# Kernel optimization log

Measured on AMD Instinct MI355X. Metric: run time of the kernel, lower is better.

Reference implementation:

```python
import jax, jax.numpy as jnp
import numpy as np

N = 20000      # vertices
KPV = 8        # key points per vertex
M = N * KPV    # total key points
E = 320000     # edges (avg in-degree 16)
KP_DIM = 4
SD = 300       # state_dim
T = 3          # GNN iterations
NC = 4         # classes
LOC = (64, 64, 7)


def _lin(key, din, dout):
    k1, k2 = jax.random.split(key)
    s = 1.0 / np.sqrt(din)
    W = jax.random.uniform(k1, (din, dout), jnp.float32, -s, s)
    b = jax.random.uniform(k2, (dout,), jnp.float32, -s, s)
    return W, b


def setup_inputs():
    key = jax.random.key(0)
    ks = jax.random.split(key, 32)
    inp = {}
    inp['key_points'] = jax.random.normal(ks[0], (M, KP_DIM), jnp.float32)
    inp['pos'] = jax.random.normal(ks[1], (N, 3), jnp.float32)
    # uniform ragged layout: vertex i owns key points [i*KPV, (i+1)*KPV)
    inp['key_points_lookup'] = jnp.arange(N, dtype=jnp.int32) * KPV
    inp['edge_index'] = jax.random.randint(ks[2], (2, E), 0, N, jnp.int32)
    # MLPInit: kp_dim -> 64 -> 128 -> state_dim (basic_block = Linear+ReLU)
    inp['Wi0'], inp['bi0'] = _lin(ks[3], KP_DIM, 64)
    inp['Wi1'], inp['bi1'] = _lin(ks[4], 64, 128)
    inp['Wi2'], inp['bi2'] = _lin(ks[5], 128, SD)
    # MLPInitAggr: state_dim -> state_dim
    inp['Wa'], inp['ba'] = _lin(ks[6], SD, SD)
    # StateConvLayer params per iteration (mlp_h: s->delta_x, mlp_f: [dx,s_j]->e, mlp_g: update)
    Wh, bh, Wf, bf, Wg, bg = [], [], [], [], [], []
    for t in range(T):
        w, b = _lin(ks[7 + 3 * t], SD, 3); Wh.append(w); bh.append(b)
        w, b = _lin(ks[8 + 3 * t], SD + 3, SD); Wf.append(w); bf.append(b)
        w, b = _lin(ks[9 + 3 * t], SD, SD); Wg.append(w); bg.append(b)
    inp['Wh'] = jnp.stack(Wh); inp['bh'] = jnp.stack(bh)
    inp['Wf'] = jnp.stack(Wf); inp['bf'] = jnp.stack(bf)
    inp['Wg'] = jnp.stack(Wg); inp['bg'] = jnp.stack(bg)
    # classification head: state_dim -> 64 -> n_classes
    inp['Wc1'], inp['bc1'] = _lin(ks[16], SD, 64)
    inp['Wc2'], inp['bc2'] = _lin(ks[17], 64, NC)
    # per-class localization heads: state_dim -> 64 -> 64 -> 7 (stacked over classes)
    Wl1, bl1, Wl2, bl2, Wl3, bl3 = [], [], [], [], [], []
    for c in range(NC):
        w, b = _lin(ks[18 + 3 * c], SD, LOC[0]); Wl1.append(w); bl1.append(b)
        w, b = _lin(ks[19 + 3 * c], LOC[0], LOC[1]); Wl2.append(w); bl2.append(b)
        w, b = _lin(ks[20 + 3 * c], LOC[1], LOC[2]); Wl3.append(w); bl3.append(b)
    inp['Wl1'] = jnp.stack(Wl1); inp['bl1'] = jnp.stack(bl1)
    inp['Wl2'] = jnp.stack(Wl2); inp['bl2'] = jnp.stack(bl2)
    inp['Wl3'] = jnp.stack(Wl3); inp['bl3'] = jnp.stack(bl3)
    return inp


def reference(key_points, pos, key_points_lookup, edge_index,
              Wi0, bi0, Wi1, bi1, Wi2, bi2, Wa, ba,
              Wh, bh, Wf, bf, Wg, bg,
              Wc1, bc1, Wc2, bc2,
              Wl1, bl1, Wl2, bl2, Wl3, bl3):
    relu = jax.nn.relu
    n = pos.shape[0]
    # ---- initial vertex state: per-key-point MLP + ragged segment-max ----
    feats = relu(key_points @ Wi0 + bi0)
    feats = relu(feats @ Wi1 + bi1)
    feats = relu(feats @ Wi2 + bi2)                      # [M, SD]
    seg = jnp.searchsorted(key_points_lookup,
                           jnp.arange(feats.shape[0], dtype=jnp.int32),
                           side='right') - 1              # key point -> vertex id
    kp_max = jax.ops.segment_max(feats, seg, num_segments=n)  # [N, SD]
    s = relu(kp_max @ Wa + ba)                            # initial vertex states
    # ---- GNN iterations (Point-GNN eqns, max aggregation) ----
    src, dst = edge_index[0], edge_index[1]
    for t in range(Wh.shape[0]):
        dx = s @ Wh[t] + bh[t]                            # [N, 3] predicted offset
        m = jnp.concatenate([pos[src] - pos[dst] + dx[dst], s[src]], axis=-1)
        e = relu(m @ Wf[t] + bf[t])                       # [E, SD] edge messages
        aggr = jax.ops.segment_max(e, dst, num_segments=n)
        aggr = jnp.where(jnp.isneginf(aggr), 0.0, aggr)   # empty segments -> 0
        s = s + (aggr @ Wg[t] + bg[t])                    # residual state update
    # ---- heads ----
    cls_pred = relu(relu(s @ Wc1 + bc1) @ Wc2 + bc2)      # [N, NC]
    h = relu(jnp.einsum('nd,cdk->cnk', s, Wl1) + bl1[:, None, :])
    h = relu(jnp.einsum('cnd,cdk->cnk', h, Wl2) + bl2[:, None, :])
    h = relu(jnp.einsum('cnd,cdk->cnk', h, Wl3) + bl3[:, None, :])  # [C, N, 7]
    reg_pred = jnp.transpose(h, (1, 0, 2)).reshape(n, -1)           # [N, C*7]
    return cls_pred, reg_pred
```

## Files before the change

kernel.cpp:

```cpp
#include <hip/hip_runtime.h>
#include <stdint.h>

#define N_V   20000
#define M_KP  160000
#define E_N   320000
#define SD    300
#define T_IT  3

typedef unsigned short bf16_t;
typedef __attribute__((ext_vector_type(8))) short short8_t;
typedef __attribute__((ext_vector_type(4))) float float4_t;

__device__ __forceinline__ float bf2f(bf16_t u) {
    return __uint_as_float(((unsigned)u) << 16);
}
__device__ __forceinline__ bf16_t f2bf(float f) {
    unsigned u = __float_as_uint(f);
    unsigned r = (u + 0x7FFFu + ((u >> 16) & 1u)) >> 16;
    return (bf16_t)r;
}

template<bool F32>
__device__ __forceinline__ float LD(const void* p, size_t i) {
    if (F32) return ((const float*)p)[i];
    return bf2f(((const bf16_t*)p)[i]);
}
template<bool F32>
__device__ __forceinline__ void ST(void* p, size_t i, float v) {
    if (F32) ((float*)p)[i] = v;
    else     ((bf16_t*)p)[i] = f2bf(v);
}
__device__ __forceinline__ float LDr(const void* p, long long i, bool f32) {
    return f32 ? ((const float*)p)[i] : bf2f(((const bf16_t*)p)[i]);
}
__device__ __forceinline__ void STr(void* p, size_t i, float v, bool f32) {
    if (f32) ((float*)p)[i] = v;
    else     ((bf16_t*)p)[i] = f2bf(v);
}

__global__ void k_detect(const unsigned* __restrict__ w, int* __restrict__ flag) {
    __shared__ int cnt_s;
    if (threadIdx.x == 0) cnt_s = 0;
    __syncthreads();
    unsigned u = w[threadIdx.x];
    unsigned lo = u & 0xFFFFu;
    int e = (lo >> 7) & 0xFF;
    int plaus = (lo == 0u) || (e >= 96 && e <= 126);
    atomicAdd(&cnt_s, plaus);
    __syncthreads();
    if (threadIdx.x == 0) flag[0] = (cnt_s >= 64) ? 0 : 1;
}

__global__ void k_zero(int* p, int n) {
    int i = blockIdx.x * blockDim.x + threadIdx.x;
    if (i < n) p[i] = 0;
}
__global__ void k_hist(const int* __restrict__ dst, int* __restrict__ cnt) {
    int e = blockIdx.x * blockDim.x + threadIdx.x;
    if (e < E_N) atomicAdd(&cnt[dst[e]], 1);
}
__global__ void k_scan(const int* __restrict__ cnt, int* __restrict__ offs,
                       int* __restrict__ cur) {
    __shared__ int buf[1024];
    __shared__ int carry_s;
    int tid = threadIdx.x;
    if (tid == 0) { carry_s = 0; offs[0] = 0; }
    __syncthreads();
    for (int base = 0; base < N_V; base += 1024) {
        int i = base + tid;
        int v = (i < N_V) ? cnt[i] : 0;
        buf[tid] = v;
        __syncthreads();
        for (int off = 1; off < 1024; off <<= 1) {
            int t = (tid >= off) ? buf[tid - off] : 0;
            __syncthreads();
            buf[tid] += t;
            __syncthreads();
        }
        int incl = buf[tid] + carry_s;
        if (i < N_V) { offs[i + 1] = incl; cur[i] = incl - v; }
        __syncthreads();
        if (tid == 1023) carry_s = incl;
        __syncthreads();
    }
}
__global__ void k_scatter(const int* __restrict__ src, const int* __restrict__ dst,
                          int* __restrict__ cur, int* __restrict__ esrc) {
    int e = blockIdx.x * blockDim.x + threadIdx.x;
    if (e < E_N) {
        int p = atomicAdd(&cur[dst[e]], 1);
        esrc[p] = src[e];
    }
}

template<bool F32>
__global__ __launch_bounds__(256) void k_init_fused(
    const void* __restrict__ kp,
    const void* __restrict__ Wi0, const void* __restrict__ bi0,
    const void* __restrict__ Wi1, const void* __restrict__ bi1,
    const void* __restrict__ Wi2, const void* __restrict__ bi2,
    float* __restrict__ kpmax, const int* __restrict__ flag) {
    if ((flag[0] != 0) != F32) return;
    __shared__ float kps[256];
    __shared__ float h1s[64][64];
    __shared__ float h2s[64 * 128];
    int tid = threadIdx.x;
    int row0 = blockIdx.x * 64;
    kps[tid] = LD<F32>(kp, (size_t)row0 * 4 + tid);
    __syncthreads();
    {
        int c = tid & 63;
        float w0 = LD<F32>(Wi0, c), w1 = LD<F32>(Wi0, 64 + c);
        float w2 = LD<F32>(Wi0, 128 + c), w3 = LD<F32>(Wi0, 192 + c);
        float b0 = LD<F32>(bi0, c);
        int rbase = (tid >> 6) * 16;
#pragma unroll
        for (int rr = 0; rr < 16; rr++) {
            int r = rbase + rr;
            float a = b0 + kps[r * 4] * w0 + kps[r * 4 + 1] * w1
                         + kps[r * 4 + 2] * w2 + kps[r * 4 + 3] * w3;
            h1s[r][c] = fmaxf(a, 0.f);
        }
    }
    __syncthreads();
    {
        int c = tid & 127;
        int rbase = (tid >> 7) * 32;
        float b1 = LD<F32>(bi1, c);
        float acc[32];
#pragma unroll
        for (int rr = 0; rr < 32; rr++) acc[rr] = b1;
        for (int k = 0; k < 64; k++) {
            float wv = LD<F32>(Wi1, (size_t)k * 128 + c);
#pragma unroll
            for (int rr = 0; rr < 32; rr++) acc[rr] += h1s[rbase + rr][k] * wv;
        }
#pragma unroll
        for (int rr = 0; rr < 32; rr++)
            h2s[(size_t)(rbase + rr) * 128 + c] = fmaxf(acc[rr], 0.f);
    }
    __syncthreads();
    {
        int cx = tid & 63, rg = tid >> 6;
        float acc[16][5];
#pragma unroll
        for (int r = 0; r < 16; r++)
#pragma unroll
            for (int j = 0; j < 5; j++) acc[r][j] = 0.f;
        bool ok4 = (cx < SD - 256);
        for (int k = 0; k < 128; k++) {
            float w[5];
#pragma unroll
            for (int j = 0; j < 4; j++) w[j] = LD<F32>(Wi2, (size_t)k * SD + cx + 64 * j);
            w[4] = ok4 ? LD<F32>(Wi2, (size_t)k * SD + cx + 256) : 0.f;
#pragma unroll
            for (int r = 0; r < 16; r++) {
                float av = h2s[(rg * 16 + r) * 128 + k];
#pragma unroll
                for (int j = 0; j < 5; j++) acc[r][j] += av * w[j];
            }
        }
        int vbase = (row0 >> 3) + rg * 2;
#pragma unroll
        for (int half = 0; half < 2; half++) {
            int v = vbase + half;
#pragma unroll
            for (int j = 0; j < 5; j++) {
                int c = cx + 64 * j;
                if (c >= SD) continue;
                float m = acc[half * 8][j];
#pragma unroll
                for (int r = 1; r < 8; r++) m = fmaxf(m, acc[half * 8 + r][j]);
                kpmax[(size_t)v * SD + c] = fmaxf(m + LD<F32>(bi2, c), 0.f);
            }
        }
    }
}

template<bool F32>
__global__ __launch_bounds__(256) void k_gemm(
    const float* __restrict__ A, const void* __restrict__ W,
    const void* __restrict__ bias, const float* res,
    float* C, int Mr, int K, int Nc, int do_relu, const int* __restrict__ flag) {
    if ((flag[0] != 0) != F32) return;
    __shared__ float As[16][65];
    __shared__ float Ws[16][64];
    int tid = threadIdx.x;
    int tx = tid & 15, ty = tid >> 4;
    int row0 = blockIdx.y * 64, col0 = blockIdx.x * 64;
    float acc[4][4] = {{0.f}};
    int lk = tid & 15, lr = tid >> 4;
    int ln = tid & 63, lk4 = tid >> 6;
    for (int k0 = 0; k0 < K; k0 += 16) {
#pragma unroll
        for (int i = 0; i < 4; i++) {
            int r = lr + i * 16;
            int gr = row0 + r, gk = k0 + lk;
            As[lk][r] = (gr < Mr && gk < K) ? A[(size_t)gr * K + gk] : 0.f;
        }
#pragma unroll
        for (int p = 0; p < 4; p++) {
            int kk = lk4 + p * 4;
            int gk = k0 + kk, gn = col0 + ln;
            Ws[kk][ln] = (gk < K && gn < Nc) ? LD<F32>(W, (size_t)gk * Nc + gn) : 0.f;
        }
        __syncthreads();
#pragma unroll
        for (int kk = 0; kk < 16; kk++) {
            float a[4], w[4];
#pragma unroll
            for (int i = 0; i < 4; i++) a[i] = As[kk][ty * 4 + i];
#pragma unroll
            for (int j = 0; j < 4; j++) w[j] = Ws[kk][tx * 4 + j];
#pragma unroll
            for (int i = 0; i < 4; i++)
#pragma unroll
                for (int j = 0; j < 4; j++) acc[i][j] += a[i] * w[j];
        }
        __syncthreads();
    }
#pragma unroll
    for (int i = 0; i < 4; i++) {
        int gr = row0 + ty * 4 + i;
        if (gr >= Mr) continue;
#pragma unroll
        for (int j = 0; j < 4; j++) {
            int gn = col0 + tx * 4 + j;
            if (gn >= Nc) continue;
            float c = acc[i][j] + LD<F32>(bias, gn);
            if (res) c += res[(size_t)gr * Nc + gn];
            if (do_relu) c = fmaxf(c, 0.f);
            C[(size_t)gr * Nc + gn] = c;
        }
    }
}

#define PREP_SPLIT 882688
#define PREP_BIAS  3104
#define PREP_TOT   (PREP_SPLIT + PREP_BIAS + 32)

__global__ __launch_bounds__(256) void k_prep(
    const void* __restrict__ Wa, const void* __restrict__ Wf,
    const void* __restrict__ Wg, const void* __restrict__ Wc1,
    const void* __restrict__ Wl1, const void* __restrict__ Wl2,
    const void* __restrict__ Wi1, const void* __restrict__ Wi2,
    const void* __restrict__ ba, const void* __restrict__ bfb,
    const void* __restrict__ bgb, const void* __restrict__ bc1,
    const void* __restrict__ bl1b, const void* __restrict__ bl2b,
    const void* __restrict__ bi1, const void* __restrict__ bi2,
    unsigned short* __restrict__ SP, float* __restrict__ biasF,
    float* __restrict__ bzero, const int* __restrict__ flag)
{
    int idx = blockIdx.x * 256 + threadIdx.x;
    if (idx >= PREP_TOT) return;
    bool f32 = flag[0] != 0;
    if (idx < PREP_SPLIT) {
        const void* src; long long eoff, cum; int srcN, Nn, Kk, Kpad, pe, local;
        if (idx < 716800) {
            int m = idx / 102400; local = idx - m * 102400;
            pe = 102400; cum = (long long)m * 102400;
            Kpad = 320; Nn = 300; Kk = 300; srcN = 300;
            src = (m == 0) ? Wa : (m <= 3 ? Wf : Wg);
            eoff = (m == 0) ? 0 : (m <= 3 ? (long long)((m - 1) * 303 + 3) * 300
                                          : (long long)(m - 4) * 90000);
        } else if (idx < 819200) {
            int j = (idx - 716800) / 20480; local = (idx - 716800) - j * 20480;
            pe = 20480; cum = 716800 + (long long)j * 20480;
            Kpad = 320; Nn = 64; Kk = 300; srcN = 64;
            src = (j == 0) ? Wc1 : Wl1;
            eoff = (j == 0) ? 0 : (long long)(j - 1) * 19200;
        } else if (idx < 835584) {
            int c = (idx - 819200) / 4096; local = (idx - 819200) - c * 4096;
            pe = 4096; cum = 819200 + (long long)c * 4096;
            Kpad = 64; Nn = 64; Kk = 64; srcN = 64;
            src = Wl2; eoff = (long long)c * 4096;
        } else if (idx < 843776) {
            local = idx - 835584;
            pe = 8192; cum = 835584;
            Kpad = 64; Nn = 128; Kk = 64; srcN = 128;
            src = Wi1; eoff = 0;
        } else {
            local = idx - 843776;
            pe = 38912; cum = 843776;
            Kpad = 128; Nn = 300; Kk = 128; srcN = 300;
            src = Wi2; eoff = 0;
        }
        int n = local / Kpad, k = local - n * Kpad;
        float v = 0.f;
        if (n < Nn && k < Kk) v = LDr(src, eoff + (long long)k * srcN + n, f32);
        bf16_t hi = f2bf(v);
        bf16_t lo = f2bf(v - bf2f(hi));
        SP[2 * cum + local] = hi;
        SP[2 * cum + pe + local] = lo;
    } else if (idx < PREP_SPLIT + PREP_BIAS) {
        int b = idx - PREP_SPLIT;
        const void* src; int o;
        if (b < 300)       { src = ba;   o = b; }
        else if (b < 1200) { src = bfb;  o = b - 300; }
        else if (b < 2100) { src = bgb;  o = b - 1200; }
        else if (b < 2164) { src = bc1;  o = b - 2100; }
        else if (b < 2420) { src = bl1b; o = b - 2164; }
        else if (b < 2676) { src = bl2b; o = b - 2420; }
        else if (b < 2804) { src = bi1;  o = b - 2676; }
        else               { src = bi2;  o = b - 2804; }
        biasF[b] = LDr(src, o, f32);
    } else {
        bzero[idx - (PREP_SPLIT + PREP_BIAS)] = 0.f;
    }
}

__device__ __forceinline__ void mfma16(float4_t& c, short8_t a, short8_t b) {
    asm("v_mfma_f32_16x16x32_bf16 %0, %1, %2, %0" : "+v"(c) : "v"(a), "v"(b));
}
__device__ __forceinline__ void split2(float a, float b, unsigned& h, unsigned& l) {
    asm("v_cvt_pk_bf16_f32 %0, %1, %2" : "=v"(h) : "v"(a), "v"(b));
    float la = a - __uint_as_float(h << 16);
    float lb = b - __uint_as_float(h & 0xFFFF0000u);
    asm("v_cvt_pk_bf16_f32 %0, %1, %2" : "=v"(l) : "v"(la), "v"(lb));
}
__device__ __forceinline__ void split8(float4_t x0, float4_t x1,
                                       short8_t* hi, short8_t* lo) {
    union { unsigned u[4]; short8_t v; } H, L;
#pragma unroll
    for (int p = 0; p < 4; p++) {
        float a, b;
        if (p == 0)      { a = x0[0]; b = x0[1]; }
        else if (p == 1) { a = x0[2]; b = x0[3]; }
        else if (p == 2) { a = x1[0]; b = x1[1]; }
        else             { a = x1[2]; b = x1[3]; }
        unsigned ph, pl;
        split2(a, b, ph, pl);
        H.u[p] = ph; L.u[p] = pl;
    }
    *hi = H.v; *lo = L.v;
}

__global__ __launch_bounds__(128) void k_init_mfma(
    const void* __restrict__ kp,
    const void* __restrict__ Wi0, const void* __restrict__ bi0,
    const unsigned short* __restrict__ W1T,
    const unsigned short* __restrict__ W2T,
    const float* __restrict__ b1F, const float* __restrict__ b2F,
    float* __restrict__ kpmax, const int* __restrict__ flag)
{
    bool f32 = flag[0] != 0;
    __shared__ __attribute__((aligned(16))) unsigned short lds[2][8704];
    int tid = threadIdx.x;
    int w = tid >> 6, lane = tid & 63;
    int l15 = lane & 15, g = lane >> 4;
    unsigned short* h2h = lds[w];
    unsigned short* h2l = lds[w] + 4352;
    int rw0 = blockIdx.x * 64 + 32 * w;

    float kpr[2][4];
#pragma unroll
    for (int mt = 0; mt < 2; mt++) {
        long long r = rw0 + mt * 16 + l15;
#pragma unroll
        for (int j = 0; j < 4; j++) kpr[mt][j] = LDr(kp, r * 4 + j, f32);
    }
    short8_t a1h[2][2], a1l[2][2];
#pragma unroll
    for (int ks = 0; ks < 2; ks++) {
        float h[2][8];
#pragma unroll
        for (int e = 0; e < 8; e++) {
            int ch = ks * 32 + 8 * g + e;
            float w0 = LDr(Wi0, ch, f32),       w1 = LDr(Wi0, 64 + ch, f32);
            float w2 = LDr(Wi0, 128 + ch, f32), w3 = LDr(Wi0, 192 + ch, f32);
            float b0 = LDr(bi0, ch, f32);
#pragma unroll
            for (int mt = 0; mt < 2; mt++)
                h[mt][e] = fmaxf(b0 + kpr[mt][0] * w0 + kpr[mt][1] * w1
                                    + kpr[mt][2] * w2 + kpr[mt][3] * w3, 0.f);
        }
#pragma unroll
        for (int mt = 0; mt < 2; mt++) {
            union { unsigned u[4]; short8_t v; } H, L;
#pragma unroll
            for (int p = 0; p < 4; p++) {
                unsigned hh, ll;
                split2(h[mt][2 * p], h[mt][2 * p + 1], hh, ll);
                H.u[p] = hh; L.u[p] = ll;
            }
            a1h[mt][ks] = H.v; a1l[mt][ks] = L.v;
        }
    }

#pragma unroll
    for (int n0 = 0; n0 < 8; n0++) {
        const unsigned short* bp = W1T + (n0 * 16 + l15) * 64 + 8 * g;
        short8_t bh0 = *(const short8_t*)bp;
        short8_t bh1 = *(const short8_t*)(bp + 32);
        short8_t bl0 = *(const short8_t*)(bp + 8192);
        short8_t bl1 = *(const short8_t*)(bp + 8224);
        float4_t c0 = {0.f, 0.f, 0.f, 0.f}, c1 = {0.f, 0.f, 0.f, 0.f};
        mfma16(c0, a1h[0][0], bh0); mfma16(c0, a1h[0][1], bh1);
        mfma16(c0, a1l[0][0], bh0); mfma16(c0, a1l[0][1], bh1);
        mfma16(c0, a1h[0][0], bl0); mfma16(c0, a1h[0][1], bl1);
        mfma16(c1, a1h[1][0], bh0); mfma16(c1, a1h[1][1], bh1);
        mfma16(c1, a1l[1][0], bh0); mfma16(c1, a1l[1][1], bh1);
        mfma16(c1, a1h[1][0], bl0); mfma16(c1, a1h[1][1], bl1);
        int col = n0 * 16 + l15;
        float bv = b1F[col];
#pragma unroll
        for (int i = 0; i < 4; i++) {
            float v0 = fmaxf(c0[i] + bv, 0.f);
            bf16_t h0 = f2bf(v0);
            h2h[(4 * g + i) * 136 + col] = h0;
            h2l[(4 * g + i) * 136 + col] = f2bf(v0 - bf2f(h0));
            float v1 = fmaxf(c1[i] + bv, 0.f);
            bf16_t h1v = f2bf(v1);
            h2h[(16 + 4 * g + i) * 136 + col] = h1v;
            h2l[(16 + 4 * g + i) * 136 + col] = f2bf(v1 - bf2f(h1v));
        }
    }
    __syncthreads();

    short8_t a2h[2][4], a2l[2][4];
#pragma unroll
    for (int mt = 0; mt < 2; mt++)
#pragma unroll
        for (int ks = 0; ks < 4; ks++) {
            int off = (mt * 16 + l15) * 136 + ks * 32 + 8 * g;
            a2h[mt][ks] = *(const short8_t*)(h2h + off);
            a2l[mt][ks] = *(const short8_t*)(h2l + off);
        }
    int vb = blockIdx.x * 8 + 4 * w;
    for (int n0 = 0; n0 < 19; n0++) {
        const unsigned short* bp = W2T + (n0 * 16 + l15) * 128 + 8 * g;
        short8_t bh[4], bl[4];
#pragma unroll
        for (int ks = 0; ks < 4; ks++) {
            bh[ks] = *(const short8_t*)(bp + ks * 32);
            bl[ks] = *(const short8_t*)(bp + 38912 + ks * 32);
        }
        float4_t c0 = {0.f, 0.f, 0.f, 0.f}, c1 = {0.f, 0.f, 0.f, 0.f};
#pragma unroll
        for (int ks = 0; ks < 4; ks++) {
            mfma16(c0, a2h[0][ks], bh[ks]); mfma16(c1, a2h[1][ks], bh[ks]);
        }
#pragma unroll
        for (int ks = 0; ks < 4; ks++) {
            mfma16(c0, a2l[0][ks], bh[ks]); mfma16(c1, a2l[1][ks], bh[ks]);
        }
#pragma unroll
        for (int ks = 0; ks < 4; ks++) {
            mfma16(c0, a2h[0][ks], bl[ks]); mfma16(c1, a2h[1][ks], bl[ks]);
        }
        float m0 = fmaxf(fmaxf(c0[0], c0[1]), fmaxf(c0[2], c0[3]));
        m0 = fmaxf(m0, __shfl_xor(m0, 16));
        float m1 = fmaxf(fmaxf(c1[0], c1[1]), fmaxf(c1[2], c1[3]));
        m1 = fmaxf(m1, __shfl_xor(m1, 16));
        int col = n0 * 16 + l15;
        if (col < SD) {
            float bv = b2F[col];
            if (g == 0) {
                kpmax[(size_t)(vb + 0) * SD + col] = fmaxf(m0 + bv, 0.f);
                kpmax[(size_t)(vb + 2) * SD + col] = fmaxf(m1 + bv, 0.f);
            } else if (g == 2) {
                kpmax[(size_t)(vb + 1) * SD + col] = fmaxf(m0 + bv, 0.f);
                kpmax[(size_t)(vb + 3) * SD + col] = fmaxf(m1 + bv, 0.f);
            }
        }
    }
}

__global__ __launch_bounds__(256) void k_gemm_mfma(
    const float* __restrict__ A, const unsigned short* __restrict__ WhiT,
    const unsigned short* __restrict__ WloT, const float* __restrict__ bias,
    const float* __restrict__ res, float* __restrict__ C,
    int M, int K, int Kpad, int N, int relu,
    long long zA, long long zW, int zB, long long zC)
{
    int z = blockIdx.z;
    A    += (size_t)z * zA;
    WhiT += (size_t)z * zW;
    WloT += (size_t)z * zW;
    bias += (size_t)z * zB;
    C    += (size_t)z * zC;
    int tid = threadIdx.x;
    int w = tid >> 6, lane = tid & 63;
    int l15 = lane & 15, g = lane >> 4;
    int row0 = blockIdx.y * 256 + w * 64;
    int col0 = blockIdx.x * 64;

    float4_t acc[4][4];
#pragma unroll
    for (int i = 0; i < 4; i++)
#pragma unroll
        for (int j = 0; j < 4; j++) acc[i][j] = (float4_t){0.f, 0.f, 0.f, 0.f};

    const unsigned short* bhp[4];
    const unsigned short* blp[4];
#pragma unroll
    for (int ns = 0; ns < 4; ns++) {
        size_t o = (size_t)(col0 + ns * 16 + l15) * Kpad + 8 * g;
        bhp[ns] = WhiT + o; blp[ns] = WloT + o;
    }
    const float* app[4];
    int amode[4]; bool adead[4];
#pragma unroll
    for (int ms = 0; ms < 4; ms++) {
        int base = row0 + ms * 16;
        int gr = base + l15;
        amode[ms] = (base + 16 <= M) ? 2 : (base < M ? 1 : 0);
        adead[ms] = gr >= M;
        int grc = gr < M ? gr : (M - 1);
        app[ms] = A + (size_t)grc * K + 8 * g;
    }
    const short8_t z8 = {0, 0, 0, 0, 0, 0, 0, 0};

    for (int k0 = 0; k0 < K; k0 += 32) {
        short8_t bh[4], bl[4], ah[4], al[4];
#pragma unroll
        for (int ns = 0; ns < 4; ns++) {
            bh[ns] = *(const short8_t*)bhp[ns]; bhp[ns] += 32;
            bl[ns] = *(const short8_t*)blp[ns]; blp[ns] += 32;
        }
#pragma unroll
        for (int ms = 0; ms < 4; ms++) {
            if (amode[ms] == 0) { ah[ms] = z8; al[ms] = z8; continue; }
            float4_t x0 = *(const float4_t*)app[ms];
            float4_t x1 = *(const float4_t*)(app[ms] + 4);
            app[ms] += 32;
            if (amode[ms] == 1 && adead[ms]) {
                x0 = (float4_t){0.f, 0.f, 0.f, 0.f};
                x1 = (float4_t){0.f, 0.f, 0.f, 0.f};
            }
            split8(x0, x1, &ah[ms], &al[ms]);
        }
#pragma unroll
        for (int ms = 0; ms < 4; ms++)
#pragma unroll
            for (int ns = 0; ns < 4; ns++) {
                mfma16(acc[ms][ns], ah[ms], bh[ns]);
                mfma16(acc[ms][ns], al[ms], bh[ns]);
                mfma16(acc[ms][ns], ah[ms], bl[ns]);
            }
    }

#pragma unroll
    for (int ns = 0; ns < 4; ns++) {
        int gn = col0 + ns * 16 + l15;
        if (gn >= N) continue;
        float bv = bias[gn];
#pragma unroll
        for (int ms = 0; ms < 4; ms++) {
            int rb = row0 + ms * 16 + 4 * g;
#pragma unroll
            for (int r = 0; r < 4; r++) {
                int gr = rb + r;
                if (gr >= M) continue;
                float c = acc[ms][ns][r] + bv;
                if (res) c += res[(size_t)gr * N + gn];
                if (relu) c = fmaxf(c, 0.f);
                C[(size_t)gr * N + gn] = c;
            }
        }
    }
}

__global__ void k_dx2(const float* __restrict__ s, const void* __restrict__ Wh,
                      const void* __restrict__ bh, int t, float* __restrict__ dx,
                      const int* __restrict__ flag) {
    bool f32 = flag[0] != 0;
    long long wo = (long long)t * SD * 3, bo = (long long)t * 3;
    int wv = threadIdx.x >> 6, lane = threadIdx.x & 63;
    int v = blockIdx.x * 4 + wv;
    if (v >= N_V) return;
    float p0 = 0.f, p1 = 0.f, p2 = 0.f;
    for (int d = lane; d < SD; d += 64) {
        float sv = s[(size_t)v * SD + d];
        p0 += sv * LDr(Wh, wo + d * 3 + 0, f32);
        p1 += sv * LDr(Wh, wo + d * 3 + 1, f32);
        p2 += sv * LDr(Wh, wo + d * 3 + 2, f32);
    }
#pragma unroll
    for (int off = 32; off > 0; off >>= 1) {
        p0 += __shfl_down(p0, off);
        p1 += __shfl_down(p1, off);
        p2 += __shfl_down(p2, off);
    }
    if (lane == 0) {
        dx[v * 3 + 0] = p0 + LDr(bh, bo + 0, f32);
        dx[v * 3 + 1] = p1 + LDr(bh, bo + 1, f32);
        dx[v * 3 + 2] = p2 + LDr(bh, bo + 2, f32);
    }
}

__global__ void k_ab2(const float* __restrict__ dx, const void* __restrict__ pos,
                      const void* __restrict__ Wf, int t, float* __restrict__ ua,
                      float* __restrict__ bbag, const int* __restrict__ flag) {
    bool f32 = flag[0] != 0;
    long long wo = (long long)t * 303 * SD;
    int idx = blockIdx.x * blockDim.x + threadIdx.x;
    if (idx >= N_V * SD) return;
    int v = idx / SD, c = idx - v * SD;
    float w0 = LDr(Wf, wo + c, f32), w1 = LDr(Wf, wo + SD + c, f32),
          w2 = LDr(Wf, wo + 2 * SD + c, f32);
    float P = LDr(pos, v * 3 + 0, f32) * w0 + LDr(pos, v * 3 + 1, f32) * w1
            + LDr(pos, v * 3 + 2, f32) * w2;
    float D = dx[v * 3 + 0] * w0 + dx[v * 3 + 1] * w1 + dx[v * 3 + 2] * w2;
    ua[idx] += P;
    bbag[idx] = D - P;
}

__global__ void k_cls2(const float* __restrict__ hc, const void* __restrict__ W,
                       const void* __restrict__ b, void* __restrict__ out,
                       const int* __restrict__ flag) {
    bool f32 = flag[0] != 0;
    int v = blockIdx.x * blockDim.x + threadIdx.x;
    if (v >= N_V) return;
    float acc[4];
#pragma unroll
    for (int j = 0; j < 4; j++) acc[j] = LDr(b, j, f32);
    for (int k = 0; k < 64; k++) {
        float h = hc[(size_t)v * 64 + k];
#pragma unroll
        for (int j = 0; j < 4; j++) acc[j] += h * LDr(W, k * 4 + j, f32);
    }
#pragma unroll
    for (int j = 0; j < 4; j++) STr(out, v * 4 + j, fmaxf(acc[j], 0.f), f32);
}

__global__ void k_loc32(const float* __restrict__ hl2all, const void* __restrict__ Wl3,
                        const void* __restrict__ bl3, void* __restrict__ out,
                        const int* __restrict__ flag) {
    bool f32 = flag[0] != 0;
    int cls = blockIdx.y;
    const float* h2 = hl2all + (size_t)cls * N_V * 64;
    long long wo = (long long)cls * 64 * 7, bo = (long long)cls * 7;
    int v = blockIdx.x * blockDim.x + threadIdx.x;
    if (v >= N_V) return;
    float acc[7];
#pragma unroll
    for (int j = 0; j < 7; j++) acc[j] = LDr(bl3, bo + j, f32);
    for (int k = 0; k < 64; k++) {
        float h = h2[(size_t)v * 64 + k];
#pragma unroll
        for (int j = 0; j < 7; j++) acc[j] += h * LDr(Wl3, wo + k * 7 + j, f32);
    }
#pragma unroll
    for (int j = 0; j < 7; j++)
        STr(out, 80000 + (size_t)v * 28 + cls * 7 + j, fmaxf(acc[j], 0.f), f32);
}

template<bool F32>
__global__ void k_dx(const float* __restrict__ s, const void* __restrict__ Wh,
                     const void* __restrict__ bh, float* __restrict__ dx,
                     const int* __restrict__ flag) {
    if ((flag[0] != 0) != F32) return;
    int wv = threadIdx.x >> 6, lane = threadIdx.x & 63;
    int v = blockIdx.x * 4 + wv;
    if (v >= N_V) return;
    float p0 = 0.f, p1 = 0.f, p2 = 0.f;
    for (int d = lane; d < SD; d += 64) {
        float sv = s[(size_t)v * SD + d];
        p0 += sv * LD<F32>(Wh, d * 3 + 0);
        p1 += sv * LD<F32>(Wh, d * 3 + 1);
        p2 += sv * LD<F32>(Wh, d * 3 + 2);
    }
#pragma unroll
    for (int off = 32; off > 0; off >>= 1) {
        p0 += __shfl_down(p0, off);
        p1 += __shfl_down(p1, off);
        p2 += __shfl_down(p2, off);
    }
    if (lane == 0) {
        dx[v * 3 + 0] = p0 + LD<F32>(bh, 0);
        dx[v * 3 + 1] = p1 + LD<F32>(bh, 1);
        dx[v * 3 + 2] = p2 + LD<F32>(bh, 2);
    }
}

template<bool F32>
__global__ void k_ab(const float* __restrict__ dx, const void* __restrict__ pos,
                     const void* __restrict__ Wf3, float* __restrict__ ua,
                     float* __restrict__ bbag, const int* __restrict__ flag) {
    if ((flag[0] != 0) != F32) return;
    int idx = blockIdx.x * blockDim.x + threadIdx.x;
    if (idx >= N_V * SD) return;
    int v = idx / SD, c = idx - v * SD;
    float w0 = LD<F32>(Wf3, c), w1 = LD<F32>(Wf3, SD + c), w2 = LD<F32>(Wf3, 2 * SD + c);
    float P = LD<F32>(pos, v * 3 + 0) * w0 + LD<F32>(pos, v * 3 + 1) * w1
            + LD<F32>(pos, v * 3 + 2) * w2;
    float D = dx[v * 3 + 0] * w0 + dx[v * 3 + 1] * w1 + dx[v * 3 + 2] * w2;
    ua[idx] += P;
    bbag[idx] = D - P;
}

__global__ __launch_bounds__(256) void k_aggr(
    const float* __restrict__ a, float* bbag,
    const int* __restrict__ offs, const int* __restrict__ esrc) {
    int wv = threadIdx.x >> 6, lane = threadIdx.x & 63;
    int v = blockIdx.x * 4 + wv;
    if (v >= N_V) return;
    int e0 = offs[v], e1 = offs[v + 1];
    float r0 = -3.0e38f, r1 = r0, r2 = r0, r3 = r0, r4 = r0;
    bool c4 = lane < SD - 256;
    for (int e = e0; e < e1; e++) {
        const float* ar = a + (size_t)esrc[e] * SD + lane;
        r0 = fmaxf(r0, ar[0]);
        r1 = fmaxf(r1, ar[64]);
        r2 = fmaxf(r2, ar[128]);
        r3 = fmaxf(r3, ar[192]);
        if (c4) r4 = fmaxf(r4, ar[256]);
    }
    float* bv = bbag + (size_t)v * SD + lane;
    bv[0]   = fmaxf(0.f, r0 + bv[0]);
    bv[64]  = fmaxf(0.f, r1 + bv[64]);
    bv[128] = fmaxf(0.f, r2 + bv[128]);
    bv[192] = fmaxf(0.f, r3 + bv[192]);
    if (c4) bv[256] = fmaxf(0.f, r4 + bv[256]);
}

template<bool F32>
__global__ void k_cls(const float* __restrict__ hc, const void* __restrict__ W,
                      const void* __restrict__ b, void* __restrict__ out,
                      const int* __restrict__ flag) {
    if ((flag[0] != 0) != F32) return;
    int v = blockIdx.x * blockDim.x + threadIdx.x;
    if (v >= N_V) return;
    float acc[4];
#pragma unroll
    for (int j = 0; j < 4; j++) acc[j] = LD<F32>(b, j);
    for (int k = 0; k < 64; k++) {
        float h = hc[(size_t)v * 64 + k];
#pragma unroll
        for (int j = 0; j < 4; j++) acc[j] += h * LD<F32>(W, k * 4 + j);
    }
#pragma unroll
    for (int j = 0; j < 4; j++) ST<F32>(out, v * 4 + j, fmaxf(acc[j], 0.f));
}

template<bool F32>
__global__ void k_loc3(const float* __restrict__ h2, const void* __restrict__ W,
                       const void* __restrict__ b, void* __restrict__ out, int cls,
                       const int* __restrict__ flag) {
    if ((flag[0] != 0) != F32) return;
    int v = blockIdx.x * blockDim.x + threadIdx.x;
    if (v >= N_V) return;
    float acc[7];
#pragma unroll
    for (int j = 0; j < 7; j++) acc[j] = LD<F32>(b, j);
    for (int k = 0; k < 64; k++) {
        float h = h2[(size_t)v * 64 + k];
#pragma unroll
        for (int j = 0; j < 7; j++) acc[j] += h * LD<F32>(W, k * 7 + j);
    }
#pragma unroll
    for (int j = 0; j < 7; j++)
        ST<F32>(out, 80000 + (size_t)v * 28 + cls * 7 + j, fmaxf(acc[j], 0.f));
}

#define LAUNCH2(kname, grid, blk, ...) \
    do { kname<false><<<grid, blk, 0, stream>>>(__VA_ARGS__); \
         kname<true><<<grid, blk, 0, stream>>>(__VA_ARGS__); } while (0)

extern "C" void kernel_launch(void* const* d_in, const int* in_sizes, int n_in,
                              void* d_out, int out_size, void* d_ws, size_t ws_size,
                              hipStream_t stream) {
    const void* kp  = d_in[0];
    const void* pos = d_in[1];
    const int* eidx = (const int*)d_in[3];
    const int* e_src = eidx;
    const int* e_dst = eidx + E_N;
    const void* Wi0 = d_in[4];   const void* bi0 = d_in[5];
    const void* Wi1 = d_in[6];   const void* bi1 = d_in[7];
    const void* Wi2 = d_in[8];   const void* bi2 = d_in[9];
    const void* Wa  = d_in[10];  const void* ba  = d_in[11];
    const char* Wh  = (const char*)d_in[12];  const char* bh = (const char*)d_in[13];
    const char* Wf  = (const char*)d_in[14];  const char* bff = (const char*)d_in[15];
    const char* Wg  = (const char*)d_in[16];  const char* bg = (const char*)d_in[17];
    const void* Wc1 = d_in[18];  const void* bc1 = d_in[19];
    const void* Wc2 = d_in[20];  const void* bc2 = d_in[21];
    const char* Wl1 = (const char*)d_in[22];  const char* bl1 = (const char*)d_in[23];
    const char* Wl2 = (const char*)d_in[24];  const char* bl2 = (const char*)d_in[25];
    const char* Wl3 = (const char*)d_in[26];  const char* bl3 = (const char*)d_in[27];

    char* ws = (char*)d_ws;
    float* regA  = (float*)(ws + 0);
    float* kpmax = regA;
    float* ua    = regA;
    float* hc    = (float*)(ws + 0);
    float* hl1m  = (float*)(ws + 0);
    float* hl1f  = (float*)(ws + 6000000);
    float* hl2f  = (float*)(ws + 12000000);
    float* bbag  = (float*)(ws + 24000000);
    float* hl2m  = (float*)(ws + 24000000);
    float* s     = (float*)(ws + 48000000);
    int*   cnt   = (int*)(ws + 72000000);
    int*   offs  = (int*)(ws + 72100000);
    int*   cur   = (int*)(ws + 72200000);
    int*   esrc  = (int*)(ws + 72300000);
    float* dx    = (float*)(ws + 73600000);
    int*   flag  = (int*)(ws + 73900000);
    unsigned short* SPLIT = (unsigned short*)(ws + 73950000);
    float* biasF = (float*)(ws + 77481000);

    bool mf = (ws_size == 0) || (ws_size >= (size_t)77500000);
    auto HI = [&](long long cum) { return SPLIT + 2 * cum; };

    k_detect<<<1, 128, 0, stream>>>((const unsigned*)Wi0, flag);

    k_zero<<<(N_V + 255) / 256, 256, 0, stream>>>(cnt, N_V);
    k_hist<<<(E_N + 255) / 256, 256, 0, stream>>>(e_dst, cnt);
    k_scan<<<1, 1024, 0, stream>>>(cnt, offs, cur);
    k_scatter<<<(E_N + 255) / 256, 256, 0, stream>>>(e_src, e_dst, cur, esrc);

    if (mf)
        k_prep<<<(PREP_TOT + 255) / 256, 256, 0, stream>>>(
            Wa, Wf, Wg, Wc1, Wl1, Wl2, Wi1, Wi2,
            ba, bff, bg, bc1, bl1, bl2, bi1, bi2,
            SPLIT, biasF, bbag, flag);

    if (mf) {
        const unsigned short* W1T = SPLIT + 2LL * 835584;
        const unsigned short* W2T = SPLIT + 2LL * 843776;
        k_init_mfma<<<M_KP / 64, 128, 0, stream>>>(kp, Wi0, bi0, W1T, W2T,
                                                   biasF + 2676, biasF + 2804,
                                                   kpmax, flag);
    } else {
        LAUNCH2(k_init_fused, M_KP / 64, 256, kp, Wi0, bi0, Wi1, bi1, Wi2, bi2, kpmax, flag);
    }

    const dim3 GSD(5, (N_V + 255) / 256);
    const dim3 G64(1, (N_V + 255) / 256);
    if (mf) {
        k_gemm_mfma<<<GSD, 256, 0, stream>>>(kpmax, HI(0), HI(0) + 102400,
                                             biasF, nullptr, s, N_V, SD, 320, SD, 1,
                                             0, 0, 0, 0);
    } else {
        dim3 g((SD + 63) / 64, (N_V + 63) / 64);
        LAUNCH2(k_gemm, g, 256, kpmax, Wa, ba, nullptr, s, N_V, SD, SD, 1, flag);
    }

    for (int t = 0; t < T_IT; t++) {
        dim3 g5((SD + 63) / 64, (N_V + 63) / 64);
        if (mf) {
            long long cum = (long long)(1 + t) * 102400;
            k_gemm_mfma<<<GSD, 256, 0, stream>>>(s, HI(cum), HI(cum) + 102400,
                                                 biasF + 300 + t * 300, nullptr, ua,
                                                 N_V, SD, 320, SD, 0, 0, 0, 0, 0);
            k_dx2<<<(N_V + 3) / 4, 256, 0, stream>>>(s, Wh, bh, t, dx, flag);
            k_ab2<<<(N_V * SD + 255) / 256, 256, 0, stream>>>(dx, pos, Wf, t, ua, bbag, flag);
        } else {
            for (int f32v = 0; f32v < 2; f32v++) {
                size_t es = f32v ? 4 : 2;
                const void* Wf_t = Wf + (size_t)t * 303 * SD * es;
                const void* WfS  = Wf + ((size_t)t * 303 + 3) * SD * es;
                const void* bf_t = bff + (size_t)t * SD * es;
                const void* Wh_t = Wh + (size_t)t * SD * 3 * es;
                const void* bh_t = bh + (size_t)t * 3 * es;
                if (f32v) {
                    k_gemm<true><<<g5, 256, 0, stream>>>(s, WfS, bf_t, nullptr, ua, N_V, SD, SD, 0, flag);
                    k_dx<true><<<(N_V + 3) / 4, 256, 0, stream>>>(s, Wh_t, bh_t, dx, flag);
                    k_ab<true><<<(N_V * SD + 255) / 256, 256, 0, stream>>>(dx, pos, Wf_t, ua, bbag, flag);
                } else {
                    k_gemm<false><<<g5, 256, 0, stream>>>(s, WfS, bf_t, nullptr, ua, N_V, SD, SD, 0, flag);
                    k_dx<false><<<(N_V + 3) / 4, 256, 0, stream>>>(s, Wh_t, bh_t, dx, flag);
                    k_ab<false><<<(N_V * SD + 255) / 256, 256, 0, stream>>>(dx, pos, Wf_t, ua, bbag, flag);
                }
            }
        }
        k_aggr<<<(N_V + 3) / 4, 256, 0, stream>>>(ua, bbag, offs, esrc);
        if (mf) {
            long long cum = (long long)(4 + t) * 102400;
            k_gemm_mfma<<<GSD, 256, 0, stream>>>(bbag, HI(cum), HI(cum) + 102400,
                                                 biasF + 1200 + t * 300, s, s,
                                                 N_V, SD, 320, SD, 0, 0, 0, 0, 0);
        } else {
            for (int f32v = 0; f32v < 2; f32v++) {
                size_t es = f32v ? 4 : 2;
                const void* Wg_t = Wg + (size_t)t * SD * SD * es;
                const void* bg_t = bg + (size_t)t * SD * es;
                if (f32v)
                    k_gemm<true><<<g5, 256, 0, stream>>>(bbag, Wg_t, bg_t, s, s, N_V, SD, SD, 0, flag);
                else
                    k_gemm<false><<<g5, 256, 0, stream>>>(bbag, Wg_t, bg_t, s, s, N_V, SD, SD, 0, flag);
            }
        }
    }

    if (mf) {
        k_gemm_mfma<<<G64, 256, 0, stream>>>(s, HI(716800), HI(716800) + 20480,
                                             biasF + 2100, nullptr, hc,
                                             N_V, SD, 320, 64, 1, 0, 0, 0, 0);
        k_cls2<<<(N_V + 255) / 256, 256, 0, stream>>>(hc, Wc2, bc2, d_out, flag);
        dim3 gz1(1, (N_V + 255) / 256, 4);
        k_gemm_mfma<<<gz1, 256, 0, stream>>>(s, HI(737280), HI(737280) + 20480,
                                             biasF + 2164, nullptr, hl1m,
                                             N_V, SD, 320, 64, 1,
                                             0, 40960, 64, 1280000);
        k_gemm_mfma<<<gz1, 256, 0, stream>>>(hl1m, HI(819200), HI(819200) + 4096,
                                             biasF + 2420, nullptr, hl2m,
                                             N_V, 64, 64, 64, 1,
                                             1280000, 8192, 64, 1280000);
        dim3 gz3((N_V + 255) / 256, 4);
        k_loc32<<<gz3, 256, 0, stream>>>(hl2m, Wl3, bl3, d_out, flag);
    } else {
        dim3 g(1, (N_V + 63) / 64);
        LAUNCH2(k_gemm, g, 256, s, Wc1, bc1, nullptr, hc, N_V, SD, 64, 1, flag);
        LAUNCH2(k_cls, (N_V + 255) / 256, 256, hc, Wc2, bc2, d_out, flag);
        for (int c = 0; c < 4; c++) {
            for (int f32v = 0; f32v < 2; f32v++) {
                size_t es = f32v ? 4 : 2;
                const void* Wl1c = Wl1 + (size_t)c * SD * 64 * es;
                const void* bl1c = bl1 + (size_t)c * 64 * es;
                const void* Wl2c = Wl2 + (size_t)c * 64 * 64 * es;
                const void* bl2c = bl2 + (size_t)c * 64 * es;
                const void* Wl3c = Wl3 + (size_t)c * 64 * 7 * es;
                const void* bl3c = bl3 + (size_t)c * 7 * es;
                if (f32v) {
                    k_gemm<true><<<g, 256, 0, stream>>>(s, Wl1c, bl1c, nullptr, hl1f, N_V, SD, 64, 1, flag);
                    k_gemm<true><<<g, 256, 0, stream>>>(hl1f, Wl2c, bl2c, nullptr, hl2f, N_V, 64, 64, 1, flag);
                    k_loc3<true><<<(N_V + 255) / 256, 256, 0, stream>>>(hl2f, Wl3c, bl3c, d_out, c, flag);
                } else {
                    k_gemm<false><<<g, 256, 0, stream>>>(s, Wl1c, bl1c, nullptr, hl1f, N_V, SD, 64, 1, flag);
                    k_gemm<false><<<g, 256, 0, stream>>>(hl1f, Wl2c, bl2c, nullptr, hl2f, N_V, 64, 64, 1, flag);
                    k_loc3<false><<<(N_V + 255) / 256, 256, 0, stream>>>(hl2f, Wl3c, bl3c, d_out, c, flag);
                }
            }
        }
    }
}
```

Measured before the change: 1.180 ms.

## Fuse edge position/offset term into message GEMM epilogue; widen init kernel blocks

The separate elementwise k_ab2 pass, which reread the whole N×300 message matrix to add the position term and wrote bbag, is folded into the epilogue of the Wf GEMM. To support this, the first three rows of Wf are pre-extracted into a float buffer during prep, and dx is computed before the GEMM. The k_init_mfma kernel also moves from 128 to 256 threads, with pairs of waves splitting the output columns of each layer. The fusion removes a full read-modify-write of a large intermediate, at the cost of extra per-element loads in the GEMM epilogue.

```diff
diff --git a/kernel.cpp b/kernel.cpp
--- a/kernel.cpp
+++ b/kernel.cpp
@@ -237,7 +237,8 @@
 
 #define PREP_SPLIT 882688
 #define PREP_BIAS  3104
-#define PREP_TOT   (PREP_SPLIT + PREP_BIAS + 32)
+#define PREP_WF3   2700
+#define PREP_TOT   (PREP_SPLIT + PREP_BIAS + PREP_WF3 + 32)
 
 __global__ __launch_bounds__(256) void k_prep(
     const void* __restrict__ Wa, const void* __restrict__ Wf,
@@ -249,6 +250,7 @@
     const void* __restrict__ bl1b, const void* __restrict__ bl2b,
     const void* __restrict__ bi1, const void* __restrict__ bi2,
     unsigned short* __restrict__ SP, float* __restrict__ biasF,
+    float* __restrict__ wf3F,
     float* __restrict__ bzero, const int* __restrict__ flag)
 {
     int idx = blockIdx.x * 256 + threadIdx.x;
@@ -304,8 +306,12 @@
         else if (b < 2804) { src = bi1;  o = b - 2676; }
         else               { src = bi2;  o = b - 2804; }
         biasF[b] = LDr(src, o, f32);
+    } else if (idx < PREP_SPLIT + PREP_BIAS + PREP_WF3) {
+        int b2 = idx - (PREP_SPLIT + PREP_BIAS);
+        int t = b2 / 900, rem = b2 - t * 900;
+        wf3F[b2] = LDr(Wf, (long long)t * 303 * SD + rem, f32);
     } else {
-        bzero[idx - (PREP_SPLIT + PREP_BIAS)] = 0.f;
+        bzero[idx - (PREP_SPLIT + PREP_BIAS + PREP_WF3)] = 0.f;
     }
 }
 
@@ -335,7 +341,7 @@
     *hi = H.v; *lo = L.v;
 }
 
-__global__ __launch_bounds__(128) void k_init_mfma(
+__global__ __launch_bounds__(256) void k_init_mfma(
     const void* __restrict__ kp,
     const void* __restrict__ Wi0, const void* __restrict__ bi0,
     const unsigned short* __restrict__ W1T,
@@ -347,10 +353,11 @@
     __shared__ __attribute__((aligned(16))) unsigned short lds[2][8704];
     int tid = threadIdx.x;
     int w = tid >> 6, lane = tid & 63;
+    int rg = w >> 1, ch = w & 1;
     int l15 = lane & 15, g = lane >> 4;
-    unsigned short* h2h = lds[w];
-    unsigned short* h2l = lds[w] + 4352;
-    int rw0 = blockIdx.x * 64 + 32 * w;
+    unsigned short* h2h = lds[rg];
+    unsigned short* h2l = lds[rg] + 4352;
+    int rw0 = blockIdx.x * 64 + rg * 32;
 
     float kpr[2][4];
 #pragma unroll
@@ -365,10 +372,10 @@
         float h[2][8];
 #pragma unroll
         for (int e = 0; e < 8; e++) {
-            int ch = ks * 32 + 8 * g + e;
-            float w0 = LDr(Wi0, ch, f32),       w1 = LDr(Wi0, 64 + ch, f32);
-            float w2 = LDr(Wi0, 128 + ch, f32), w3 = LDr(Wi0, 192 + ch, f32);
-            float b0 = LDr(bi0, ch, f32);
+            int chn = ks * 32 + 8 * g + e;
+            float w0 = LDr(Wi0, chn, f32),       w1 = LDr(Wi0, 64 + chn, f32);
+            float w2 = LDr(Wi0, 128 + chn, f32), w3 = LDr(Wi0, 192 + chn, f32);
+            float b0 = LDr(bi0, chn, f32);
 #pragma unroll
             for (int mt = 0; mt < 2; mt++)
                 h[mt][e] = fmaxf(b0 + kpr[mt][0] * w0 + kpr[mt][1] * w1
@@ -388,7 +395,8 @@
     }
 
 #pragma unroll
-    for (int n0 = 0; n0 < 8; n0++) {
+    for (int i = 0; i < 4; i++) {
+        int n0 = ch * 4 + i;
         const unsigned short* bp = W1T + (n0 * 16 + l15) * 64 + 8 * g;
         short8_t bh0 = *(const short8_t*)bp;
         short8_t bh1 = *(const short8_t*)(bp + 32);
@@ -404,15 +412,15 @@
         int col = n0 * 16 + l15;
         float bv = b1F[col];
 #pragma unroll
-        for (int i = 0; i < 4; i++) {
-            float v0 = fmaxf(c0[i] + bv, 0.f);
+        for (int i2 = 0; i2 < 4; i2++) {
+            float v0 = fmaxf(c0[i2] + bv, 0.f);
             bf16_t h0 = f2bf(v0);
-            h2h[(4 * g + i) * 136 + col] = h0;
-            h2l[(4 * g + i) * 136 + col] = f2bf(v0 - bf2f(h0));
-            float v1 = fmaxf(c1[i] + bv, 0.f);
+            h2h[(4 * g + i2) * 136 + col] = h0;
+            h2l[(4 * g + i2) * 136 + col] = f2bf(v0 - bf2f(h0));
+            float v1 = fmaxf(c1[i2] + bv, 0.f);
             bf16_t h1v = f2bf(v1);
-            h2h[(16 + 4 * g + i) * 136 + col] = h1v;
-            h2l[(16 + 4 * g + i) * 136 + col] = f2bf(v1 - bf2f(h1v));
+            h2h[(16 + 4 * g + i2) * 136 + col] = h1v;
+            h2l[(16 + 4 * g + i2) * 136 + col] = f2bf(v1 - bf2f(h1v));
         }
     }
     __syncthreads();
@@ -426,8 +434,9 @@
             a2h[mt][ks] = *(const short8_t*)(h2h + off);
             a2l[mt][ks] = *(const short8_t*)(h2l + off);
         }
-    int vb = blockIdx.x * 8 + 4 * w;
-    for (int n0 = 0; n0 < 19; n0++) {
+    int vb = blockIdx.x * 8 + rg * 4;
+    int n0beg = ch ? 10 : 0, n0end = ch ? 19 : 10;
+    for (int n0 = n0beg; n0 < n0end; n0++) {
         const unsigned short* bp = W2T + (n0 * 16 + l15) * 128 + 8 * g;
         short8_t bh[4], bl[4];
 #pragma unroll
@@ -471,7 +480,9 @@
     const unsigned short* __restrict__ WloT, const float* __restrict__ bias,
     const float* __restrict__ res, float* __restrict__ C,
     int M, int K, int Kpad, int N, int relu,
-    long long zA, long long zW, int zB, long long zC)
+    long long zA, long long zW, int zB, long long zC,
+    const void* posp, const float* dxv, const float* wf3F,
+    float* bbag, const int* __restrict__ flag)
 {
     int z = blockIdx.z;
     A    += (size_t)z * zA;
@@ -540,11 +551,15 @@
             }
     }
 
+    bool ab = posp != nullptr;
+    bool pf32 = ab && (flag[0] != 0);
 #pragma unroll
     for (int ns = 0; ns < 4; ns++) {
         int gn = col0 + ns * 16 + l15;
         if (gn >= N) continue;
         float bv = bias[gn];
+        float w30 = 0.f, w31 = 0.f, w32 = 0.f;
+        if (ab) { w30 = wf3F[gn]; w31 = wf3F[300 + gn]; w32 = wf3F[600 + gn]; }
 #pragma unroll
         for (int ms = 0; ms < 4; ms++) {
             int rb = row0 + ms * 16 + 4 * g;
@@ -553,6 +568,15 @@
                 int gr = rb + r;
                 if (gr >= M) continue;
                 float c = acc[ms][ns][r] + bv;
+                if (ab) {
+                    float P = LDr(posp, (long long)gr * 3 + 0, pf32) * w30
+                            + LDr(posp, (long long)gr * 3 + 1, pf32) * w31
+                            + LDr(posp, (long long)gr * 3 + 2, pf32) * w32;
+                    float D = dxv[gr * 3 + 0] * w30 + dxv[gr * 3 + 1] * w31
+                            + dxv[gr * 3 + 2] * w32;
+                    c += P;
+                    bbag[(size_t)gr * N + gn] = D - P;
+                }
                 if (res) c += res[(size_t)gr * N + gn];
                 if (relu) c = fmaxf(c, 0.f);
                 C[(size_t)gr * N + gn] = c;
@@ -587,23 +611,6 @@
         dx[v * 3 + 1] = p1 + LDr(bh, bo + 1, f32);
         dx[v * 3 + 2] = p2 + LDr(bh, bo + 2, f32);
     }
-}
-
-__global__ void k_ab2(const float* __restrict__ dx, const void* __restrict__ pos,
-                      const void* __restrict__ Wf, int t, float* __restrict__ ua,
-                      float* __restrict__ bbag, const int* __restrict__ flag) {
-    bool f32 = flag[0] != 0;
-    long long wo = (long long)t * 303 * SD;
-    int idx = blockIdx.x * blockDim.x + threadIdx.x;
-    if (idx >= N_V * SD) return;
-    int v = idx / SD, c = idx - v * SD;
-    float w0 = LDr(Wf, wo + c, f32), w1 = LDr(Wf, wo + SD + c, f32),
-          w2 = LDr(Wf, wo + 2 * SD + c, f32);
-    float P = LDr(pos, v * 3 + 0, f32) * w0 + LDr(pos, v * 3 + 1, f32) * w1
-            + LDr(pos, v * 3 + 2, f32) * w2;
-    float D = dx[v * 3 + 0] * w0 + dx[v * 3 + 1] * w1 + dx[v * 3 + 2] * w2;
-    ua[idx] += P;
-    bbag[idx] = D - P;
 }
 
 __global__ void k_cls2(const float* __restrict__ hc, const void* __restrict__ W,
@@ -795,6 +802,7 @@
     int*   cur   = (int*)(ws + 72200000);
     int*   esrc  = (int*)(ws + 72300000);
     float* dx    = (float*)(ws + 73600000);
+    float* wf3F  = (float*)(ws + 73844000);
     int*   flag  = (int*)(ws + 73900000);
     unsigned short* SPLIT = (unsigned short*)(ws + 73950000);
     float* biasF = (float*)(ws + 77481000);
@@ -813,12 +821,12 @@
         k_prep<<<(PREP_TOT + 255) / 256, 256, 0, stream>>>(
             Wa, Wf, Wg, Wc1, Wl1, Wl2, Wi1, Wi2,
             ba, bff, bg, bc1, bl1, bl2, bi1, bi2,
-            SPLIT, biasF, bbag, flag);
+            SPLIT, biasF, wf3F, bbag, flag);
 
     if (mf) {
         const unsigned short* W1T = SPLIT + 2LL * 835584;
         const unsigned short* W2T = SPLIT + 2LL * 843776;
-        k_init_mfma<<<M_KP / 64, 128, 0, stream>>>(kp, Wi0, bi0, W1T, W2T,
+        k_init_mfma<<<M_KP / 64, 256, 0, stream>>>(kp, Wi0, bi0, W1T, W2T,
                                                    biasF + 2676, biasF + 2804,
                                                    kpmax, flag);
     } else {
@@ -830,7 +838,8 @@
     if (mf) {
         k_gemm_mfma<<<GSD, 256, 0, stream>>>(kpmax, HI(0), HI(0) + 102400,
                                              biasF, nullptr, s, N_V, SD, 320, SD, 1,
-                                             0, 0, 0, 0);
+                                             0, 0, 0, 0,
+                                             nullptr, nullptr, nullptr, nullptr, nullptr);
     } else {
         dim3 g((SD + 63) / 64, (N_V + 63) / 64);
         LAUNCH2(k_gemm, g, 256, kpmax, Wa, ba, nullptr, s, N_V, SD, SD, 1, flag);
@@ -839,12 +848,12 @@
     for (int t = 0; t < T_IT; t++) {
         dim3 g5((SD + 63) / 64, (N_V + 63) / 64);
         if (mf) {
+            k_dx2<<<(N_V + 3) / 4, 256, 0, stream>>>(s, Wh, bh, t, dx, flag);
             long long cum = (long long)(1 + t) * 102400;
             k_gemm_mfma<<<GSD, 256, 0, stream>>>(s, HI(cum), HI(cum) + 102400,
                                                  biasF + 300 + t * 300, nullptr, ua,
-                                                 N_V, SD, 320, SD, 0, 0, 0, 0, 0);
-            k_dx2<<<(N_V + 3) / 4, 256, 0, stream>>>(s, Wh, bh, t, dx, flag);
-            k_ab2<<<(N_V * SD + 255) / 256, 256, 0, stream>>>(dx, pos, Wf, t, ua, bbag, flag);
+                                                 N_V, SD, 320, SD, 0, 0, 0, 0, 0,
+                                                 pos, dx, wf3F + t * 900, bbag, flag);
         } else {
             for (int f32v = 0; f32v < 2; f32v++) {
                 size_t es = f32v ? 4 : 2;
@@ -869,7 +878,8 @@
             long long cum = (long long)(4 + t) * 102400;
             k_gemm_mfma<<<GSD, 256, 0, stream>>>(bbag, HI(cum), HI(cum) + 102400,
                                                  biasF + 1200 + t * 300, s, s,
-                                                 N_V, SD, 320, SD, 0, 0, 0, 0, 0);
+                                                 N_V, SD, 320, SD, 0, 0, 0, 0, 0,
+                                                 nullptr, nullptr, nullptr, nullptr, nullptr);
         } else {
             for (int f32v = 0; f32v < 2; f32v++) {
                 size_t es = f32v ? 4 : 2;
@@ -886,17 +896,20 @@
     if (mf) {
         k_gemm_mfma<<<G64, 256, 0, stream>>>(s, HI(716800), HI(716800) + 20480,
                                              biasF + 2100, nullptr, hc,
-                                             N_V, SD, 320, 64, 1, 0, 0, 0, 0);
+                                             N_V, SD, 320, 64, 1, 0, 0, 0, 0,
+                                             nullptr, nullptr, nullptr, nullptr, nullptr);
         k_cls2<<<(N_V + 255) / 256, 256, 0, stream>>>(hc, Wc2, bc2, d_out, flag);
         dim3 gz1(1, (N_V + 255) / 256, 4);
         k_gemm_mfma<<<gz1, 256, 0, stream>>>(s, HI(737280), HI(737280) + 20480,
                                              biasF + 2164, nullptr, hl1m,
                                              N_V, SD, 320, 64, 1,
-                                             0, 40960, 64, 1280000);
+                                             0, 40960, 64, 1280000,
+                                             nullptr, nullptr, nullptr, nullptr, nullptr);
         k_gemm_mfma<<<gz1, 256, 0, stream>>>(hl1m, HI(819200), HI(819200) + 4096,
                                              biasF + 2420, nullptr, hl2m,
                                              N_V, 64, 64, 64, 1,
-                                             1280000, 8192, 64, 1280000);
+                                             1280000, 8192, 64, 1280000,
+                                             nullptr, nullptr, nullptr, nullptr, nullptr);
         dim3 gz3((N_V + 255) / 256, 4);
         k_loc32<<<gz3, 256, 0, stream>>>(hl2m, Wl3, bl3, d_out, flag);
     } else {
```

Result: no change. 1.190 ms (+0.8%).
